# Kernel tuning notes

Hardware: AMD Instinct MI355X
Metric: run time of the kernel (lower is better)

Reference implementation:

```python
import jax, jax.numpy as jnp
import numpy as np
import math

H, D, HD = 4, 32, 128      # heads, head dim, hidden
N = 100000                 # nodes per node type
E = 200000                 # edges per edge type
L = 2                      # HGT layers
ET = [(0, 1), (1, 0), (1, 1)]  # (src_type, dst_type) for edge types r2s, s2r, s2s
SQRT_D = math.sqrt(D)


def setup_inputs() -> dict:
    key = jax.random.key(0)
    ks = jax.random.split(key, 20)
    f = lambda k, shape, s=0.05: jax.random.normal(k, shape, dtype=jnp.float32) * s
    return {
        "x_region": f(ks[0], (N, 64), 1.0),
        "x_site": f(ks[1], (N, 32), 1.0),
        "proj_W_region": f(ks[2], (64, HD)),
        "proj_b_region": jnp.zeros((HD,), jnp.float32),
        "proj_W_site": f(ks[3], (32, HD)),
        "proj_b_site": jnp.zeros((HD,), jnp.float32),
        # per-layer, per-node-type k/q/v and output projections (node types: 0=region, 1=site)
        "Wk": f(ks[4], (L, 2, HD, HD)),
        "bk": f(ks[5], (L, 2, HD)),
        "Wq": f(ks[6], (L, 2, HD, HD)),
        "bq": f(ks[7], (L, 2, HD)),
        "Wv": f(ks[8], (L, 2, HD, HD)),
        "bv": f(ks[9], (L, 2, HD)),
        "Wo": f(ks[10], (L, 2, HD, HD)),
        "bo": f(ks[11], (L, 2, HD)),
        "skip": jnp.ones((L, 2), jnp.float32),  # learnable skip gate logits
        # per-layer, per-edge-type, per-head relation transforms and priors
        "Krel": f(ks[12], (L, 3, H, D, D), 0.1),
        "Vrel": f(ks[13], (L, 3, H, D, D), 0.1),
        "prel": jnp.ones((L, 3, H), jnp.float32),
        "edge_r2s": jax.random.randint(ks[14], (2, E), 0, N),
        "edge_s2r": jax.random.randint(ks[15], (2, E), 0, N),
        "edge_s2s": jax.random.randint(ks[16], (2, E), 0, N),
    }


def _hgt_conv(xs, edges, Wk, bk, Wq, bq, Wv, bv, Wo, bo, skip, Krel, Vrel, prel):
    # xs: list of [N, HD] per node type; edges: list of [2, E] per edge type
    k = [(xs[t] @ Wk[t] + bk[t]).reshape(-1, H, D) for t in range(2)]
    q = [(xs[t] @ Wq[t] + bq[t]).reshape(-1, H, D) for t in range(2)]
    v = [(xs[t] @ Wv[t] + bv[t]).reshape(-1, H, D) for t in range(2)]
    buckets = {0: [], 1: []}  # incoming messages grouped by dst node type
    for r, (s, d) in enumerate(ET):
        src, dst = edges[r][0], edges[r][1]
        kt = jnp.einsum('nhd,hde->nhe', k[s], Krel[r])[src]  # [E,H,D]
        vt = jnp.einsum('nhd,hde->nhe', v[s], Vrel[r])[src]  # [E,H,D]
        sc = jnp.sum(q[d][dst] * kt, axis=-1) * (prel[r] / SQRT_D)  # [E,H]
        buckets[d].append((sc, vt, dst))
    out = []
    for t in range(2):
        sc = jnp.concatenate([b[0] for b in buckets[t]], axis=0)
        vv = jnp.concatenate([b[1] for b in buckets[t]], axis=0)
        dd = jnp.concatenate([b[2] for b in buckets[t]], axis=0)
        # segment softmax over all incoming edges of each destination node
        m = jax.ops.segment_max(sc, dd, num_segments=N)
        e = jnp.exp(sc - m[dd])
        den = jax.ops.segment_sum(e, dd, num_segments=N)
        alpha = e / den[dd]
        msg = jax.ops.segment_sum(alpha[:, :, None] * vv, dd, num_segments=N).reshape(N, HD)
        o = jax.nn.gelu(msg, approximate=False) @ Wo[t] + bo[t]
        a = jax.nn.sigmoid(skip[t])
        out.append(a * o + (1.0 - a) * xs[t])
    return out


def reference(x_region, x_site, proj_W_region, proj_b_region, proj_W_site, proj_b_site,
              Wk, bk, Wq, bq, Wv, bv, Wo, bo, skip, Krel, Vrel, prel,
              edge_r2s, edge_s2r, edge_s2s):
    xs = [x_region @ proj_W_region + proj_b_region,
          x_site @ proj_W_site + proj_b_site]
    edges = [edge_r2s, edge_s2r, edge_s2s]
    for l in range(L):
        hs = _hgt_conv(xs, edges, Wk[l], bk[l], Wq[l], bq[l], Wv[l], bv[l],
                       Wo[l], bo[l], skip[l], Krel[l], Vrel[l], prel[l])
        xs = [jax.nn.relu(h) for h in hs]  # post_proj is Identity (128//4*4 == 128)
    return (xs[0], xs[1])
```

## Files before the change

kernel.cpp:

```cpp
#include <hip/hip_runtime.h>
#include <hip/hip_bf16.h>

#define HD 128
#define H 4
#define D 32
#define SLOTS 64

typedef __hip_bfloat16 bf16;
typedef __attribute__((ext_vector_type(8))) short bf16x8;
typedef __attribute__((ext_vector_type(4))) float f32x4;
typedef __attribute__((ext_vector_type(4))) short short4v;

__device__ __forceinline__ float bf2f(unsigned short u) {
    union { unsigned int i; float f; } v; v.i = ((unsigned int)u) << 16; return v.f;
}
__device__ __forceinline__ short f2bf(float f) {
    union { float f; unsigned u; } v; v.f = f;
    unsigned r = v.u + 0x7fff + ((v.u >> 16) & 1);
    return (short)(r >> 16);
}
__device__ __forceinline__ short4v pack4(float a0, float a1, float a2, float a3) {
    union { unsigned u[2]; short4v v; } r;
    asm("v_cvt_pk_bf16_f32 %0, %1, %2" : "=v"(r.u[0]) : "v"(a0), "v"(a1));
    asm("v_cvt_pk_bf16_f32 %0, %1, %2" : "=v"(r.u[1]) : "v"(a2), "v"(a3));
    return r.v;
}
__device__ __forceinline__ bf16x8 pack8(const f32x4 lo, const f32x4 hi) {
    union { unsigned u[4]; bf16x8 v; } r;
    asm("v_cvt_pk_bf16_f32 %0, %1, %2" : "=v"(r.u[0]) : "v"(lo[0]), "v"(lo[1]));
    asm("v_cvt_pk_bf16_f32 %0, %1, %2" : "=v"(r.u[1]) : "v"(lo[2]), "v"(lo[3]));
    asm("v_cvt_pk_bf16_f32 %0, %1, %2" : "=v"(r.u[2]) : "v"(hi[0]), "v"(hi[1]));
    asm("v_cvt_pk_bf16_f32 %0, %1, %2" : "=v"(r.u[3]) : "v"(hi[2]), "v"(hi[3]));
    return r.v;
}

__global__ __launch_bounds__(256) void transpose_bf16(
    const float* __restrict__ src, bf16* __restrict__ dst, int K, int C, int Kd, int total) {
    int i = blockIdx.x * 256 + threadIdx.x;
    if (i >= total) return;
    int kd = i % Kd; int rem = i / Kd; int c = rem % C; int b = rem / C;
    float v = (kd < K) ? src[((size_t)b * K + kd) * C + c] : 0.f;
    ((unsigned short*)dst)[i] = (unsigned short)f2bf(v);
}

__global__ __launch_bounds__(256) void fuse_relw(
    const float* __restrict__ Wk, const float* __restrict__ Wv,
    const float* __restrict__ Krel, const float* __restrict__ Vrel,
    bf16* __restrict__ Wall) {
    int gid = blockIdx.x * 256 + threadIdx.x;
    int m = gid >> 14;
    int idx = gid & 16383;
    int ep = idx >> 7, i = idx & 127;
    int l = m / 6, kv = (m / 3) & 1, r = m % 3;
    int s = (r == 0) ? 0 : 1;
    const float* W = (kv ? Wv : Wk) + ((size_t)(l * 2 + s)) * 16384;
    const float* R = (kv ? Vrel : Krel) + ((size_t)(l * 3 + r)) * 4096;
    int h = ep >> 5, e = ep & 31;
    float acc = 0.f;
#pragma unroll
    for (int d = 0; d < 32; ++d)
        acc = fmaf(W[i * 128 + h * 32 + d], R[h * 1024 + d * 32 + e], acc);
    int slot = l * 8 + 2 + kv * 3 + r;
    ((unsigned short*)Wall)[(size_t)slot * 16384 + ep * 128 + i] = (unsigned short)f2bf(acc);
}

__global__ __launch_bounds__(256) void fuse_relb(
    const float* __restrict__ bk, const float* __restrict__ bv, const float* __restrict__ bq,
    const float* __restrict__ Krel, const float* __restrict__ Vrel,
    float* __restrict__ Ball) {
    int gid = blockIdx.x * 256 + threadIdx.x;
    if (gid >= 2048) return;
    int col = gid & 127, m = gid >> 7;
    int l = m >> 3, g = m & 7;
    float val;
    if (g < 2) {
        val = bq[(l * 2 + g) * 128 + col];
    } else {
        int kv = (g - 2) / 3, r = (g - 2) % 3, s = (r == 0) ? 0 : 1;
        const float* b = (kv ? bv : bk) + (size_t)(l * 2 + s) * 128;
        const float* R = (kv ? Vrel : Krel) + (size_t)(l * 3 + r) * 4096;
        int h = col >> 5, e = col & 31;
        float acc = 0.f;
#pragma unroll
        for (int d = 0; d < 32; ++d)
            acc = fmaf(b[h * 32 + d], R[h * 1024 + d * 32 + e], acc);
        val = acc;
    }
    Ball[gid] = val;
}

__global__ __launch_bounds__(256) void build_adj(
    const int* __restrict__ edge, int* __restrict__ adj, int* __restrict__ deg,
    int dstBase, int rel, int E) {
    int i = blockIdx.x * 256 + threadIdx.x;
    if (i >= E) return;
    int src = edge[i];
    int dst = edge[E + i];
    int slot = atomicAdd(deg + dstBase + dst, 1);
    if (slot < SLOTS) adj[(size_t)(dstBase + dst) * SLOTS + slot] = src | (rel << 20);
}


__device__ __forceinline__ void qkv_phase(
    const short* Xs, const bf16* __restrict__ Wall, const float* __restrict__ Ball,
    bf16* __restrict__ qo, bf16* __restrict__ kvo,
    int t, int n0, int N, int w, int l16, int lgrp) {
    size_t NB = (size_t)N * HD;
    int nsl = t ? 5 : 3;
    unsigned list = t ? 0x76431u : 0x520u;
    for (int si = 0; si < nsl; ++si) {
        int g = (list >> (4 * si)) & 15;
        const bf16* WT = Wall + (size_t)g * 16384;
        bf16x8 Wc[2][4];
#pragma unroll
        for (int c2 = 0; c2 < 2; ++c2)
#pragma unroll
            for (int kk = 0; kk < 4; ++kk)
                Wc[c2][kk] = *(const bf16x8*)&WT[((w * 2 + c2) * 16 + l16) * 128 + kk * 32 + lgrp * 8];
        const float* bb = Ball + g * 128;
        f32x4 bv0 = *(const f32x4*)&bb[(w * 2 + 0) * 16 + lgrp * 4];
        f32x4 bv1 = *(const f32x4*)&bb[(w * 2 + 1) * 16 + lgrp * 4];
        f32x4 acc[8][2];
#pragma unroll
        for (int rt = 0; rt < 8; ++rt) { acc[rt][0] = bv0; acc[rt][1] = bv1; }
#pragma unroll
        for (int rt = 0; rt < 8; ++rt) {
#pragma unroll
            for (int kk = 0; kk < 4; ++kk) {
                bf16x8 xb = *(const bf16x8*)&Xs[(rt * 16 + l16) * 136 + kk * 32 + lgrp * 8];
                acc[rt][0] = __builtin_amdgcn_mfma_f32_16x16x32_bf16(Wc[0][kk], xb, acc[rt][0], 0, 0, 0);
                acc[rt][1] = __builtin_amdgcn_mfma_f32_16x16x32_bf16(Wc[1][kk], xb, acc[rt][1], 0, 0, 0);
            }
        }
        unsigned short* outp;
        int rowStride, off2;
        if (g < 2) {
            outp = (unsigned short*)(qo + (size_t)g * NB);
            rowStride = HD; off2 = 0;
        } else {
            int gi = g - 2, r = gi % 3, isV = gi / 3;
            outp = (unsigned short*)(kvo + (size_t)r * N * 256);
            rowStride = 256; off2 = isV * 128;
        }
#pragma unroll
        for (int rt = 0; rt < 8; ++rt) {
            int node = n0 + rt * 16 + l16;
            if (node < N) {
#pragma unroll
                for (int c2 = 0; c2 < 2; ++c2) {
                    short4v s = pack4(acc[rt][c2][0], acc[rt][c2][1], acc[rt][c2][2], acc[rt][c2][3]);
                    *(short4v*)(outp + (size_t)node * rowStride + off2 + (w * 2 + c2) * 16 + lgrp * 4) = s;
                }
            }
        }
    }
}

__global__ __launch_bounds__(256) void proj_qkv(
    const float* __restrict__ xr, const float* __restrict__ xsi,
    const bf16* __restrict__ WrT, const float* __restrict__ br,
    const bf16* __restrict__ WsT, const float* __restrict__ bs,
    bf16* __restrict__ xsb,
    const bf16* __restrict__ Wall, const float* __restrict__ Ball,
    bf16* __restrict__ qo, bf16* __restrict__ kvo, int N, int nb0) {
    __shared__ short Xs[128 * 136];
    int b = blockIdx.x;
    int t = b < nb0 ? 1 : 0;
    int blk = t ? b : b - nb0;
    int tid = threadIdx.x;
    int w = tid >> 6, lane = tid & 63, l16 = lane & 15, lgrp = lane >> 4;
    int n0 = blk * 128;
    int rowbase = n0 + w * 32;
    int K = t ? 32 : 64;
    const float* X = t ? xsi : xr;
    const bf16* WT = t ? WsT : WrT;
    const float* bb = t ? bs : br;
    f32x4 acc[2][8];
#pragma unroll
    for (int c = 0; c < 8; ++c) {
        f32x4 bv = *(const f32x4*)&bb[c * 16 + lgrp * 4];
        acc[0][c] = bv; acc[1][c] = bv;
    }
    int r0 = rowbase + l16, r1 = rowbase + 16 + l16;
    bool v0 = r0 < N, v1 = r1 < N;
    size_t b0 = (size_t)(v0 ? r0 : 0) * K, b1 = (size_t)(v1 ? r1 : 0) * K;
    int nkk = K >> 5;
    for (int kk = 0; kk < nkk; ++kk) {
        int ko = kk * 32 + lgrp * 8;
        f32x4 lo0 = {0,0,0,0}, hi0 = {0,0,0,0}, lo1 = {0,0,0,0}, hi1 = {0,0,0,0};
        if (v0) { lo0 = *(const f32x4*)&X[b0 + ko]; hi0 = *(const f32x4*)&X[b0 + ko + 4]; }
        if (v1) { lo1 = *(const f32x4*)&X[b1 + ko]; hi1 = *(const f32x4*)&X[b1 + ko + 4]; }
        bf16x8 x0 = pack8(lo0, hi0);
        bf16x8 x1 = pack8(lo1, hi1);
#pragma unroll
        for (int c = 0; c < 8; ++c) {
            bf16x8 wa = *(const bf16x8*)&WT[(size_t)(c * 16 + l16) * K + ko];
            acc[0][c] = __builtin_amdgcn_mfma_f32_16x16x32_bf16(wa, x0, acc[0][c], 0, 0, 0);
            acc[1][c] = __builtin_amdgcn_mfma_f32_16x16x32_bf16(wa, x1, acc[1][c], 0, 0, 0);
        }
    }
#pragma unroll
    for (int nt = 0; nt < 2; ++nt) {
        int lrow = w * 32 + nt * 16 + l16;
        int node = n0 + lrow;
        bool vn = node < N;
#pragma unroll
        for (int c = 0; c < 8; ++c) {
            int col = c * 16 + lgrp * 4;
            short4v s = pack4(acc[nt][c][0], acc[nt][c][1], acc[nt][c][2], acc[nt][c][3]);
            if (vn) *(short4v*)((unsigned short*)xsb + ((size_t)t * N + node) * HD + col) = s;
            *(short4v*)&Xs[lrow * 136 + col] = s;
        }
    }
    __syncthreads();
    qkv_phase(Xs, Wall, Ball, qo, kvo, t, n0, N, w, l16, lgrp);
}

__global__ __launch_bounds__(256) void gather_kernel(
    const int* __restrict__ adj, const int* __restrict__ deg,
    const bf16* __restrict__ q, const bf16* __restrict__ kv,
    const float* __restrict__ prel, bf16* __restrict__ g, int N2, int N) {
    int grp = (blockIdx.x * 256 + threadIdx.x) >> 5;
    int lane = threadIdx.x & 31;
    if (grp >= N2) return;
    int h = lane >> 3;

    ushort4 qa = *((const ushort4*)(q + (size_t)grp * HD) + lane);
    float q0 = bf2f(qa.x), q1 = bf2f(qa.y), q2 = bf2f(qa.z), q3 = bf2f(qa.w);
    const float is = 0.17677669529663687f;
    float pr0 = prel[0 * H + h] * is, pr1 = prel[1 * H + h] * is, pr2 = prel[2 * H + h] * is;

    float m0 = 0.f, m1 = 0.f, m2 = 0.f, m3 = 0.f, dacc = 0.f;
    int dg = deg[grp]; if (dg > SLOTS) dg = SLOTS;
    const int* lst = adj + (size_t)grp * SLOTS;
    int myeA = (lane < dg) ? lst[lane] : 0;
    int myeB = (lane + 32 < dg) ? lst[lane + 32] : 0;

    if (dg > 0) {
        int ecur = __shfl(myeA, 0, 32);
        const bf16* base = kv + ((size_t)(ecur >> 20) * N + (ecur & 0xFFFFF)) * 256;
        ushort4 ka = *((const ushort4*)base + lane);
        ushort4 va = *((const ushort4*)base + 32 + lane);
        for (int i = 0; i < dg; ++i) {
            int en = 0;
            ushort4 kan = {0, 0, 0, 0}, van = {0, 0, 0, 0};
            if (i + 1 < dg) {
                en = (i + 1 < 32) ? __shfl(myeA, i + 1, 32) : __shfl(myeB, i + 1 - 32, 32);
                const bf16* basen = kv + ((size_t)(en >> 20) * N + (en & 0xFFFFF)) * 256;
                kan = *((const ushort4*)basen + lane);
                van = *((const ushort4*)basen + 32 + lane);
            }
            int r = ecur >> 20;
            float p = q0 * bf2f(ka.x) + q1 * bf2f(ka.y) + q2 * bf2f(ka.z) + q3 * bf2f(ka.w);
            p += __shfl_xor(p, 1);
            p += __shfl_xor(p, 2);
            p += __shfl_xor(p, 4);
            float prv = (r == 0) ? pr0 : ((r == 1) ? pr1 : pr2);
            float eh = __expf(p * prv);
            m0 = fmaf(eh, bf2f(va.x), m0);
            m1 = fmaf(eh, bf2f(va.y), m1);
            m2 = fmaf(eh, bf2f(va.z), m2);
            m3 = fmaf(eh, bf2f(va.w), m3);
            dacc += eh;
            ecur = en; ka = kan; va = van;
        }
    }
    float inv = dacc > 0.f ? 1.f / dacc : 0.f;
    const float c = 0.70710678118654752f;
    float v0 = m0 * inv, v1 = m1 * inv, v2 = m2 * inv, v3 = m3 * inv;
    float g0 = 0.5f * v0 * (1.f + erff(v0 * c));
    float g1 = 0.5f * v1 * (1.f + erff(v1 * c));
    float g2 = 0.5f * v2 * (1.f + erff(v2 * c));
    float g3 = 0.5f * v3 * (1.f + erff(v3 * c));
    *((short4v*)(g + (size_t)grp * HD) + lane) = pack4(g0, g1, g2, g3);
}

__global__ __launch_bounds__(256) void out_qkv(
    bf16* __restrict__ xsb, const bf16* __restrict__ gbuf,
    const bf16* __restrict__ WoT, const float* __restrict__ bo,
    const float* __restrict__ skip,
    const bf16* __restrict__ Wall, const float* __restrict__ Ball,
    bf16* __restrict__ qo, bf16* __restrict__ kvo, int N, int nb0) {
    __shared__ short S[128 * 136];
    int b = blockIdx.x;
    int t = b < nb0 ? 1 : 0;
    int blk = t ? b : b - nb0;
    int tid = threadIdx.x;
    int w = tid >> 6, lane = tid & 63, l16 = lane & 15, lgrp = lane >> 4;
    int n0 = blk * 128;
    size_t NB = (size_t)N * HD;
    const bf16* G = gbuf + (size_t)t * NB;
#pragma unroll
    for (int j = 0; j < 8; ++j) {
        int flat = tid + j * 256;
        int row = flat >> 4, c16 = flat & 15;
        bf16x8 v = {0, 0, 0, 0, 0, 0, 0, 0};
        if (n0 + row < N) v = *(const bf16x8*)&G[(size_t)(n0 + row) * HD + c16 * 8];
        *(bf16x8*)&S[row * 136 + c16 * 8] = v;
    }
    __syncthreads();
    const bf16* WT = WoT + (size_t)t * 16384;
    bf16x8 Wc[2][4];
#pragma unroll
    for (int c2 = 0; c2 < 2; ++c2)
#pragma unroll
        for (int kk = 0; kk < 4; ++kk)
            Wc[c2][kk] = *(const bf16x8*)&WT[((w * 2 + c2) * 16 + l16) * 128 + kk * 32 + lgrp * 8];
    const float* bb = bo + t * 128;
    f32x4 bv0 = *(const f32x4*)&bb[(w * 2 + 0) * 16 + lgrp * 4];
    f32x4 bv1 = *(const f32x4*)&bb[(w * 2 + 1) * 16 + lgrp * 4];
    f32x4 acc[8][2];
#pragma unroll
    for (int rt = 0; rt < 8; ++rt) { acc[rt][0] = bv0; acc[rt][1] = bv1; }
#pragma unroll
    for (int rt = 0; rt < 8; ++rt) {
#pragma unroll
        for (int kk = 0; kk < 4; ++kk) {
            bf16x8 xb = *(const bf16x8*)&S[(rt * 16 + l16) * 136 + kk * 32 + lgrp * 8];
            acc[rt][0] = __builtin_amdgcn_mfma_f32_16x16x32_bf16(Wc[0][kk], xb, acc[rt][0], 0, 0, 0);
            acc[rt][1] = __builtin_amdgcn_mfma_f32_16x16x32_bf16(Wc[1][kk], xb, acc[rt][1], 0, 0, 0);
        }
    }
    float a = 1.f / (1.f + expf(-skip[t]));
    short4v pv[8][2];
#pragma unroll
    for (int rt = 0; rt < 8; ++rt) {
        int node = n0 + rt * 16 + l16;
        size_t base = ((size_t)t * N + (size_t)(node < N ? node : 0)) * HD;
#pragma unroll
        for (int c2 = 0; c2 < 2; ++c2)
            pv[rt][c2] = *(const short4v*)((const unsigned short*)xsb + base + (w * 2 + c2) * 16 + lgrp * 4);
    }
    __syncthreads();
#pragma unroll
    for (int rt = 0; rt < 8; ++rt) {
        int lrow = rt * 16 + l16;
        int node = n0 + lrow;
        bool vn = node < N;
#pragma unroll
        for (int c2 = 0; c2 < 2; ++c2) {
            int col = (w * 2 + c2) * 16 + lgrp * 4;
            short4v s;
            if (vn) {
                size_t idx = ((size_t)t * N + node) * HD + col;
                f32x4 o;
#pragma unroll
                for (int j = 0; j < 4; ++j)
                    o[j] = fmaxf(a * acc[rt][c2][j] + (1.f - a) * bf2f((unsigned short)pv[rt][c2][j]), 0.f);
                s = pack4(o[0], o[1], o[2], o[3]);
                *(short4v*)((unsigned short*)xsb + idx) = s;
            } else {
                s = (short4v){0, 0, 0, 0};
            }
            *(short4v*)&S[lrow * 136 + col] = s;
        }
    }
    __syncthreads();
    qkv_phase(S, Wall, Ball, qo, kvo, t, n0, N, w, l16, lgrp);
}

__global__ __launch_bounds__(256) void out_gemm(
    float* __restrict__ xs, const bf16* __restrict__ xsb, const bf16* __restrict__ gbuf,
    const bf16* __restrict__ WoT, const float* __restrict__ bo,
    const float* __restrict__ skip, int N, int nb0) {
    __shared__ short Gs[128 * 136];
    int b = blockIdx.x;
    int t = b >= nb0 ? 1 : 0;
    int blk = t ? b - nb0 : b;
    int tid = threadIdx.x;
    int w = tid >> 6, lane = tid & 63, l16 = lane & 15, lgrp = lane >> 4;
    int n0 = blk * 128;
    size_t NB = (size_t)N * HD;
    const bf16* G = gbuf + (size_t)t * NB;
#pragma unroll
    for (int j = 0; j < 8; ++j) {
        int flat = tid + j * 256;
        int row = flat >> 4, c16 = flat & 15;
        bf16x8 v = {0, 0, 0, 0, 0, 0, 0, 0};
        if (n0 + row < N) v = *(const bf16x8*)&G[(size_t)(n0 + row) * HD + c16 * 8];
        *(bf16x8*)&Gs[row * 136 + c16 * 8] = v;
    }
    __syncthreads();
    const bf16* WT = WoT + (size_t)t * 16384;
    bf16x8 Wc[2][4];
#pragma unroll
    for (int c2 = 0; c2 < 2; ++c2)
#pragma unroll
        for (int kk = 0; kk < 4; ++kk)
            Wc[c2][kk] = *(const bf16x8*)&WT[((w * 2 + c2) * 16 + l16) * 128 + kk * 32 + lgrp * 8];
    const float* bb = bo + t * 128;
    f32x4 bv0 = *(const f32x4*)&bb[(w * 2 + 0) * 16 + lgrp * 4];
    f32x4 bv1 = *(const f32x4*)&bb[(w * 2 + 1) * 16 + lgrp * 4];
    f32x4 acc[8][2];
#pragma unroll
    for (int rt = 0; rt < 8; ++rt) { acc[rt][0] = bv0; acc[rt][1] = bv1; }
#pragma unroll
    for (int rt = 0; rt < 8; ++rt) {
#pragma unroll
        for (int kk = 0; kk < 4; ++kk) {
            bf16x8 xb = *(const bf16x8*)&Gs[(rt * 16 + l16) * 136 + kk * 32 + lgrp * 8];
            acc[rt][0] = __builtin_amdgcn_mfma_f32_16x16x32_bf16(Wc[0][kk], xb, acc[rt][0], 0, 0, 0);
            acc[rt][1] = __builtin_amdgcn_mfma_f32_16x16x32_bf16(Wc[1][kk], xb, acc[rt][1], 0, 0, 0);
        }
    }
    float a = 1.f / (1.f + expf(-skip[t]));
    short4v pv[8][2];
#pragma unroll
    for (int rt = 0; rt < 8; ++rt) {
        int node = n0 + rt * 16 + l16;
        size_t base = ((size_t)t * N + (size_t)(node < N ? node : 0)) * HD;
#pragma unroll
        for (int c2 = 0; c2 < 2; ++c2)
            pv[rt][c2] = *(const short4v*)((const unsigned short*)xsb + base + (w * 2 + c2) * 16 + lgrp * 4);
    }
#pragma unroll
    for (int rt = 0; rt < 8; ++rt) {
        int node = n0 + rt * 16 + l16;
        if (node < N) {
#pragma unroll
            for (int c2 = 0; c2 < 2; ++c2) {
                size_t idx = ((size_t)t * N + node) * HD + (w * 2 + c2) * 16 + lgrp * 4;
                f32x4 o;
#pragma unroll
                for (int j = 0; j < 4; ++j)
                    o[j] = fmaxf(a * acc[rt][c2][j] + (1.f - a) * bf2f((unsigned short)pv[rt][c2][j]), 0.f);
                *(f32x4*)&xs[idx] = o;
            }
        }
    }
}

extern "C" void kernel_launch(void* const* d_in, const int* in_sizes, int n_in,
                              void* d_out, int out_size, void* d_ws, size_t ws_size,
                              hipStream_t stream) {
    const float* x_region = (const float*)d_in[0];
    const float* x_site   = (const float*)d_in[1];
    const float* pWr  = (const float*)d_in[2];
    const float* pbr  = (const float*)d_in[3];
    const float* pWs  = (const float*)d_in[4];
    const float* pbs  = (const float*)d_in[5];
    const float* Wk   = (const float*)d_in[6];
    const float* bk   = (const float*)d_in[7];
    const float* Wq   = (const float*)d_in[8];
    const float* bq   = (const float*)d_in[9];
    const float* Wv   = (const float*)d_in[10];
    const float* bv   = (const float*)d_in[11];
    const float* Wo   = (const float*)d_in[12];
    const float* bo   = (const float*)d_in[13];
    const float* skip = (const float*)d_in[14];
    const float* Krel = (const float*)d_in[15];
    const float* Vrel = (const float*)d_in[16];
    const float* prel = (const float*)d_in[17];
    const int* e0 = (const int*)d_in[18];
    const int* e1 = (const int*)d_in[19];
    const int* e2 = (const int*)d_in[20];

    int N = in_sizes[0] / 64;
    int E = in_sizes[18] / 2;
    int nb0 = (N + 127) / 128;
    int N2 = 2 * N;

    float* xs = (float*)d_out;

    size_t NB = (size_t)N * HD;
    char* p = (char*)d_ws;
    bf16* q_bf  = (bf16*)p; p += 2 * NB * sizeof(bf16);
    bf16* kv_bf = (bf16*)p; p += 3 * (size_t)N * 256 * sizeof(bf16);
    bf16* g_bf  = (bf16*)p; p += 2 * NB * sizeof(bf16);
    bf16* xsb   = (bf16*)p; p += 2 * NB * sizeof(bf16);
    int*  adj   = (int*)p;  p += (size_t)N2 * SLOTS * sizeof(int);
    int*  deg   = (int*)p;  p += (size_t)N2 * sizeof(int);
    bf16* PWrT  = (bf16*)p; p += 8192 * sizeof(bf16);
    bf16* PWsT  = (bf16*)p; p += 4096 * sizeof(bf16);
    bf16* Wall  = (bf16*)p; p += 2 * 8 * 16384 * sizeof(bf16);
    bf16* WoT_a = (bf16*)p; p += 2 * 2 * 16384 * sizeof(bf16);
    float* Ball = (float*)p; p += 2 * 8 * 128 * sizeof(float);
    (void)ws_size; (void)n_in; (void)out_size;

    hipMemsetAsync(deg, 0, (size_t)N2 * sizeof(int), stream);
    int bgrid = (E + 255) / 256;
    build_adj<<<bgrid, 256, 0, stream>>>(e0, adj, deg, N, 0, E);
    build_adj<<<bgrid, 256, 0, stream>>>(e1, adj, deg, 0, 1, E);
    build_adj<<<bgrid, 256, 0, stream>>>(e2, adj, deg, N, 2, E);

    transpose_bf16<<<32, 256, 0, stream>>>(pWr, PWrT, 64, 128, 64, 8192);
    transpose_bf16<<<16, 256, 0, stream>>>(pWs, PWsT, 32, 128, 32, 4096);
    for (int l = 0; l < 2; ++l) {
        transpose_bf16<<<128, 256, 0, stream>>>(Wq + (size_t)l * 2 * 16384,
                                                Wall + (size_t)l * 8 * 16384, 128, 128, 128, 32768);
        transpose_bf16<<<128, 256, 0, stream>>>(Wo + (size_t)l * 2 * 16384,
                                                WoT_a + (size_t)l * 2 * 16384, 128, 128, 128, 32768);
    }
    fuse_relw<<<768, 256, 0, stream>>>(Wk, Wv, Krel, Vrel, Wall);
    fuse_relb<<<8, 256, 0, stream>>>(bk, bv, bq, Krel, Vrel, Ball);

    int ggrid = (N2 * 32 + 255) / 256;

    proj_qkv<<<2 * nb0, 256, 0, stream>>>(
        x_region, x_site, PWrT, pbr, PWsT, pbs, xsb,
        Wall, Ball, q_bf, kv_bf, N, nb0);
    gather_kernel<<<ggrid, 256, 0, stream>>>(
        adj, deg, q_bf, kv_bf, prel, g_bf, N2, N);
    out_qkv<<<2 * nb0, 256, 0, stream>>>(
        xsb, g_bf, WoT_a, bo, skip,
        Wall + (size_t)8 * 16384, Ball + 8 * 128, q_bf, kv_bf, N, nb0);
    gather_kernel<<<ggrid, 256, 0, stream>>>(
        adj, deg, q_bf, kv_bf, prel + 12, g_bf, N2, N);
    out_gemm<<<2 * nb0, 256, 0, stream>>>(
        xs, xsb, g_bf, WoT_a + (size_t)2 * 16384, bo + 2 * HD, skip + 2, N, nb0);
}
```

Baseline: 541.3 us.

## Use full 64-lane wavefront per destination node in gather kernel

```diff
diff --git a/kernel.cpp b/kernel.cpp
--- a/kernel.cpp
+++ b/kernel.cpp
@@ -220,12 +220,12 @@
     const int* __restrict__ adj, const int* __restrict__ deg,
     const bf16* __restrict__ q, const bf16* __restrict__ kv,
     const float* __restrict__ prel, bf16* __restrict__ g, int N2, int N) {
-    int grp = (blockIdx.x * 256 + threadIdx.x) >> 5;
-    int lane = threadIdx.x & 31;
+    int grp = (blockIdx.x * 256 + threadIdx.x) >> 6;
+    int lane = threadIdx.x & 63;
     if (grp >= N2) return;
-    int h = lane >> 3;
-
-    ushort4 qa = *((const ushort4*)(q + (size_t)grp * HD) + lane);
+    int h = (lane & 31) >> 3;
+
+    ushort4 qa = *((const ushort4*)(q + (size_t)grp * HD) + (lane & 31));
     float q0 = bf2f(qa.x), q1 = bf2f(qa.y), q2 = bf2f(qa.z), q3 = bf2f(qa.w);
     const float is = 0.17677669529663687f;
     float pr0 = prel[0 * H + h] * is, pr1 = prel[1 * H + h] * is, pr2 = prel[2 * H + h] * is;
@@ -233,46 +233,46 @@
     float m0 = 0.f, m1 = 0.f, m2 = 0.f, m3 = 0.f, dacc = 0.f;
     int dg = deg[grp]; if (dg > SLOTS) dg = SLOTS;
     const int* lst = adj + (size_t)grp * SLOTS;
-    int myeA = (lane < dg) ? lst[lane] : 0;
-    int myeB = (lane + 32 < dg) ? lst[lane + 32] : 0;
+    int mye = (lane < dg) ? lst[lane] : 0;
 
     if (dg > 0) {
-        int ecur = __shfl(myeA, 0, 32);
+        int ecur = __shfl(mye, 0);
         const bf16* base = kv + ((size_t)(ecur >> 20) * N + (ecur & 0xFFFFF)) * 256;
-        ushort4 ka = *((const ushort4*)base + lane);
-        ushort4 va = *((const ushort4*)base + 32 + lane);
+        ushort4 ra = *((const ushort4*)base + lane);
         for (int i = 0; i < dg; ++i) {
             int en = 0;
-            ushort4 kan = {0, 0, 0, 0}, van = {0, 0, 0, 0};
+            ushort4 ran = {0, 0, 0, 0};
             if (i + 1 < dg) {
-                en = (i + 1 < 32) ? __shfl(myeA, i + 1, 32) : __shfl(myeB, i + 1 - 32, 32);
+                en = __shfl(mye, i + 1);
                 const bf16* basen = kv + ((size_t)(en >> 20) * N + (en & 0xFFFFF)) * 256;
-                kan = *((const ushort4*)basen + lane);
-                van = *((const ushort4*)basen + 32 + lane);
+                ran = *((const ushort4*)basen + lane);
             }
             int r = ecur >> 20;
-            float p = q0 * bf2f(ka.x) + q1 * bf2f(ka.y) + q2 * bf2f(ka.z) + q3 * bf2f(ka.w);
+            float p = q0 * bf2f(ra.x) + q1 * bf2f(ra.y) + q2 * bf2f(ra.z) + q3 * bf2f(ra.w);
             p += __shfl_xor(p, 1);
             p += __shfl_xor(p, 2);
             p += __shfl_xor(p, 4);
+            p = __shfl(p, lane & 31);
             float prv = (r == 0) ? pr0 : ((r == 1) ? pr1 : pr2);
             float eh = __expf(p * prv);
-            m0 = fmaf(eh, bf2f(va.x), m0);
-            m1 = fmaf(eh, bf2f(va.y), m1);
-            m2 = fmaf(eh, bf2f(va.z), m2);
-            m3 = fmaf(eh, bf2f(va.w), m3);
+            m0 = fmaf(eh, bf2f(ra.x), m0);
+            m1 = fmaf(eh, bf2f(ra.y), m1);
+            m2 = fmaf(eh, bf2f(ra.z), m2);
+            m3 = fmaf(eh, bf2f(ra.w), m3);
             dacc += eh;
-            ecur = en; ka = kan; va = van;
-        }
-    }
-    float inv = dacc > 0.f ? 1.f / dacc : 0.f;
-    const float c = 0.70710678118654752f;
-    float v0 = m0 * inv, v1 = m1 * inv, v2 = m2 * inv, v3 = m3 * inv;
-    float g0 = 0.5f * v0 * (1.f + erff(v0 * c));
-    float g1 = 0.5f * v1 * (1.f + erff(v1 * c));
-    float g2 = 0.5f * v2 * (1.f + erff(v2 * c));
-    float g3 = 0.5f * v3 * (1.f + erff(v3 * c));
-    *((short4v*)(g + (size_t)grp * HD) + lane) = pack4(g0, g1, g2, g3);
+            ecur = en; ra = ran;
+        }
+    }
+    if (lane >= 32) {
+        float inv = dacc > 0.f ? 1.f / dacc : 0.f;
+        const float c = 0.70710678118654752f;
+        float v0 = m0 * inv, v1 = m1 * inv, v2 = m2 * inv, v3 = m3 * inv;
+        float g0 = 0.5f * v0 * (1.f + erff(v0 * c));
+        float g1 = 0.5f * v1 * (1.f + erff(v1 * c));
+        float g2 = 0.5f * v2 * (1.f + erff(v2 * c));
+        float g3 = 0.5f * v3 * (1.f + erff(v3 * c));
+        *((short4v*)(g + (size_t)grp * HD) + (lane - 32)) = pack4(g0, g1, g2, g3);
+    }
 }
 
 __global__ __launch_bounds__(256) void out_qkv(
@@ -494,7 +494,7 @@
     fuse_relw<<<768, 256, 0, stream>>>(Wk, Wv, Krel, Vrel, Wall);
     fuse_relb<<<8, 256, 0, stream>>>(bk, bv, bq, Krel, Vrel, Ball);
 
-    int ggrid = (N2 * 32 + 255) / 256;
+    int ggrid = ((size_t)N2 * 64 + 255) / 256;
 
     proj_qkv<<<2 * nb0, 256, 0, stream>>>(
         x_region, x_site, PWrT, pbr, PWsT, pbs, xsb,
```

Result: slower. 608.2 us (+12.4%).
